# Optimization experiments

Hardware: AMD Instinct MI355X
Metric: run time of the kernel (lower is better)

Reference implementation:

```python
import jax, jax.numpy as jnp
import numpy as np

B, D, E = 8192, 4096, 64
TOP_K = 2
NOISE_EPSILON = 0.01


def setup_inputs() -> dict:
    key = jax.random.key(0)
    k1, k2, k3, k4 = jax.random.split(key, 4)
    return {
        "x": jax.random.normal(k1, (B, D), dtype=jnp.float32),
        # nn.Linear weights, init std=0.1, no bias; torch stores [out, in]
        "gate_w": jax.random.normal(k2, (E, D), dtype=jnp.float32) * 0.1,
        "noise_gate_w": jax.random.normal(k3, (E, D), dtype=jnp.float32) * 0.1,
        # deterministic stand-in for torch.randn_like(clean_logits)
        "noise": jax.random.normal(k4, (B, E), dtype=jnp.float32),
    }


def reference(x, gate_w, noise_gate_w, noise):
    # clean_logits = x @ W_g^T : [B, E]
    clean_logits = jnp.einsum("bd,ed->be", x, gate_w)
    # training path: noisy logits with softplus-scaled noise
    noise_logits = jnp.einsum("bd,ed->be", x, noise_gate_w)
    noisy_logits = clean_logits + noise * jax.nn.softplus(noise_logits) * NOISE_EPSILON
    # top-k over experts, softmax over the k selected logits
    top_k_logits, top_k_indices = jax.lax.top_k(noisy_logits, TOP_K)  # [B, k]
    top_k_gates = jax.nn.softmax(top_k_logits, axis=-1)
    # scatter back into dense [B, E] gates
    rows = jnp.arange(noisy_logits.shape[0])[:, None]  # [B, 1]
    gates = jnp.zeros_like(noisy_logits).at[rows, top_k_indices].set(top_k_gates)
    load = jax.nn.softmax(clean_logits, axis=-1)
    return (gates, load)
```

## Files before the change

### kernel.cpp

```cpp
#include <hip/hip_runtime.h>
#include <math.h>

#define BB 8192
#define DD 4096
#define EE 64

constexpr float NOISE_EPS = 0.01f;
constexpr int BM  = 64;
constexpr int BK  = 32;

typedef __attribute__((ext_vector_type(8))) _Float16 f16x8;
typedef __attribute__((ext_vector_type(4))) float    f32x4;

__device__ __forceinline__ void split8(const float4& a, const float4& b,
                                       f16x8& hi, f16x8& mi) {
    float v[8] = {a.x, a.y, a.z, a.w, b.x, b.y, b.z, b.w};
    #pragma unroll
    for (int j = 0; j < 8; ++j) {
        _Float16 h = (_Float16)v[j];
        hi[j] = h;
        mi[j] = (_Float16)(v[j] - (float)h);
    }
}

__device__ __forceinline__ void gl_lds16(const void* g, void* l) {
    __builtin_amdgcn_global_load_lds(
        (const __attribute__((address_space(1))) unsigned*)g,
        (__attribute__((address_space(3))) unsigned*)l, 16, 0, 0);
}

__global__ __launch_bounds__(256) void wsplit_pack(
    const float* __restrict__ gw, const float* __restrict__ ngw,
    char* __restrict__ wpk)
{
    const int gid = blockIdx.x * 256 + threadIdx.x;
    const int r   = gid >> 9;
    const int kc  = gid & 511;
    const int k0  = kc * 8;
    const float* src = (r < EE) ? gw + (size_t)r * DD + k0
                                : ngw + (size_t)(r - EE) * DD + k0;
    float4 a = *reinterpret_cast<const float4*>(src);
    float4 b = *reinterpret_cast<const float4*>(src + 4);
    f16x8 hi, mi;
    split8(a, b, hi, mi);
    const int T    = k0 >> 5;
    const int kq   = (k0 >> 3) & 3;
    const int cb   = r >> 4;
    const int lane = kq * 16 + (r & 15);
    char* base = wpk + (size_t)T * 16384;
    *reinterpret_cast<f16x8*>(base + ((cb * 2 + 0) * 64 + lane) * 16) = hi;
    *reinterpret_cast<f16x8*>(base + ((cb * 2 + 1) * 64 + lane) * 16) = mi;
}

template <int SK>
__global__ __launch_bounds__(512, 4) void gating_main(
    const float* __restrict__ x,
    const char*  __restrict__ wpk,
    float* __restrict__ partial)
{
    constexpr int KC  = DD / SK;
    constexpr int NKS = KC / BK;

    __shared__ __align__(1024) char xbuf[4][8192];

    const int tid  = threadIdx.x;
    const int bid  = blockIdx.x;
    const int sk   = bid & (SK - 1);
    const int row0 = (bid / SK) * BM;
    const int lane = tid & 63;
    const int wv   = tid >> 6;
    const int m2   = wv & 1;
    const int n2   = wv >> 1;
    const int l15  = lane & 15;
    const int kq   = lane >> 4;

    const int xrow = tid >> 3;
    const int xch  = tid & 7;
    const float* xg = x + (size_t)(row0 + xrow) * DD + sk * KC
                        + ((xch ^ (xrow & 7)) << 2);
    const int ldst = wv * 1024;
    char* xls = (char*)&xbuf[0][0];

    int xoff[2][2];
    #pragma unroll
    for (int mb = 0; mb < 2; ++mb) {
        const int ar = m2 * 32 + mb * 16 + l15;
        #pragma unroll
        for (int u = 0; u < 2; ++u)
            xoff[mb][u] = ar * 128 + (((kq * 2 + u) ^ (ar & 7)) << 4);
    }

    const char* wgB = wpk + ((size_t)(sk * NKS) << 14) + lane * 16;
    const int off_h0 = ((n2 * 2 + 0) * 2 + 0) * 1024;
    const int off_m0 = ((n2 * 2 + 0) * 2 + 1) * 1024;
    const int off_h1 = ((n2 * 2 + 1) * 2 + 0) * 1024;
    const int off_m1 = ((n2 * 2 + 1) * 2 + 1) * 1024;

    f32x4 acc00 = {0.f,0.f,0.f,0.f}, acc01 = {0.f,0.f,0.f,0.f};
    f32x4 acc10 = {0.f,0.f,0.f,0.f}, acc11 = {0.f,0.f,0.f,0.f};

    #define LOADB(t, BH0, BM0, BH1, BM1) do {                                  \
        const char* _b = wgB + ((size_t)(t) << 14);                            \
        BH0 = *reinterpret_cast<const f16x8*>(_b + off_h0);                    \
        BM0 = *reinterpret_cast<const f16x8*>(_b + off_m0);                    \
        BH1 = *reinterpret_cast<const f16x8*>(_b + off_h1);                    \
        BM1 = *reinterpret_cast<const f16x8*>(_b + off_m1);                    \
    } while (0)

    #define COMPUTE(t, BH0, BM0, BH1, BM1) do {                                \
        const char* _xb = xls + (((t) & 3) << 13);                             \
        float4 a00 = *reinterpret_cast<const float4*>(_xb + xoff[0][0]);       \
        float4 a01 = *reinterpret_cast<const float4*>(_xb + xoff[0][1]);       \
        float4 a10 = *reinterpret_cast<const float4*>(_xb + xoff[1][0]);       \
        float4 a11 = *reinterpret_cast<const float4*>(_xb + xoff[1][1]);       \
        f16x8 ah0, am0, ah1, am1;                                              \
        split8(a00, a01, ah0, am0);                                            \
        split8(a10, a11, ah1, am1);                                            \
        acc00 = __builtin_amdgcn_mfma_f32_16x16x32_f16(ah0, BH0, acc00, 0,0,0);\
        acc01 = __builtin_amdgcn_mfma_f32_16x16x32_f16(ah0, BH1, acc01, 0,0,0);\
        acc10 = __builtin_amdgcn_mfma_f32_16x16x32_f16(ah1, BH0, acc10, 0,0,0);\
        acc11 = __builtin_amdgcn_mfma_f32_16x16x32_f16(ah1, BH1, acc11, 0,0,0);\
        acc00 = __builtin_amdgcn_mfma_f32_16x16x32_f16(am0, BH0, acc00, 0,0,0);\
        acc01 = __builtin_amdgcn_mfma_f32_16x16x32_f16(am0, BH1, acc01, 0,0,0);\
        acc10 = __builtin_amdgcn_mfma_f32_16x16x32_f16(am1, BH0, acc10, 0,0,0);\
        acc11 = __builtin_amdgcn_mfma_f32_16x16x32_f16(am1, BH1, acc11, 0,0,0);\
        acc00 = __builtin_amdgcn_mfma_f32_16x16x32_f16(ah0, BM0, acc00, 0,0,0);\
        acc01 = __builtin_amdgcn_mfma_f32_16x16x32_f16(ah0, BM1, acc01, 0,0,0);\
        acc10 = __builtin_amdgcn_mfma_f32_16x16x32_f16(ah1, BM0, acc10, 0,0,0);\
        acc11 = __builtin_amdgcn_mfma_f32_16x16x32_f16(ah1, BM1, acc11, 0,0,0);\
    } while (0)

    f16x8 pH0, pM0, pH1, pM1;
    f16x8 qH0, qM0, qH1, qM1;

    gl_lds16(xg,            xls + ldst);
    gl_lds16(xg + BK,       xls + 8192 + ldst);
    gl_lds16(xg + 2 * BK,   xls + 16384 + ldst);
    LOADB(0, pH0, pM0, pH1, pM1);
    asm volatile("s_waitcnt vmcnt(0)" ::: "memory");
    __builtin_amdgcn_s_barrier();

    for (int t = 0; t < NKS; t += 2) {
        {
            const int tb = (t + 1 < NKS) ? t + 1 : NKS - 1;
            LOADB(tb, qH0, qM0, qH1, qM1);
            asm volatile("s_waitcnt vmcnt(5)" ::: "memory");
            __builtin_amdgcn_s_barrier();
            const int tx = (t + 3 < NKS) ? t + 3 : NKS - 1;
            gl_lds16(xg + (size_t)tx * BK, xls + (((t + 3) & 3) << 13) + ldst);
            COMPUTE(t, pH0, pM0, pH1, pM1);
        }
        {
            const int tb = (t + 2 < NKS) ? t + 2 : NKS - 1;
            LOADB(tb, pH0, pM0, pH1, pM1);
            asm volatile("s_waitcnt vmcnt(5)" ::: "memory");
            __builtin_amdgcn_s_barrier();
            const int tx = (t + 4 < NKS) ? t + 4 : NKS - 1;
            gl_lds16(xg + (size_t)tx * BK, xls + (((t + 4) & 3) << 13) + ldst);
            COMPUTE(t + 1, qH0, qM0, qH1, qM1);
        }
    }
    asm volatile("s_waitcnt vmcnt(0)" ::: "memory");

    #undef LOADB
    #undef COMPUTE

    const size_t pbase = ((size_t)sk * BB + row0) * 128;
    #pragma unroll
    for (int j = 0; j < 4; ++j) {
        const int r0 = m2 * 32 + kq * 4 + j;
        const int c0 = n2 * 32 + l15;
        partial[pbase + (size_t)r0 * 128 + c0]             = acc00[j];
        partial[pbase + (size_t)r0 * 128 + c0 + 16]        = acc01[j];
        partial[pbase + (size_t)(r0 + 16) * 128 + c0]      = acc10[j];
        partial[pbase + (size_t)(r0 + 16) * 128 + c0 + 16] = acc11[j];
    }
}

template <int SK>
__global__ __launch_bounds__(512) void gating_epi(
    const float* __restrict__ partial,
    const float* __restrict__ noise,
    float* __restrict__ out)
{
    const int tid  = threadIdx.x;
    const int wv   = tid >> 6;
    const int lane = tid & 63;
    const int l15  = lane & 15;
    const int kq   = lane >> 4;
    const int grow = blockIdx.x * 32 + wv * 4 + kq;
    const int s    = l15;

    const float* pb = partial + (size_t)grow * 128 + 4 * s;
    float4 c4 = {0.f,0.f,0.f,0.f}, n4 = {0.f,0.f,0.f,0.f};
    #pragma unroll
    for (int k = 0; k < SK; ++k) {
        const float* p = pb + (size_t)k * BB * 128;
        float4 a = *reinterpret_cast<const float4*>(p);
        float4 b = *reinterpret_cast<const float4*>(p + 64);
        c4.x += a.x; c4.y += a.y; c4.z += a.z; c4.w += a.w;
        n4.x += b.x; n4.y += b.y; n4.z += b.z; n4.w += b.w;
    }

    float4 nz = *reinterpret_cast<const float4*>(noise + (size_t)grow * EE + 4 * s);

    float cc[4] = {c4.x, c4.y, c4.z, c4.w};
    float nl[4] = {n4.x, n4.y, n4.z, n4.w};
    float m1 = -3.4e38f, m2 = -3.4e38f;
    int   i1 = -1, i2 = -1;
    float cmax = -3.4e38f;
    #pragma unroll
    for (int j = 0; j < 4; ++j) {
        const int e = 4 * s + j;
        float sp  = fmaxf(nl[j], 0.0f) + log1pf(expf(-fabsf(nl[j])));
        float nzj = (j == 0) ? nz.x : (j == 1) ? nz.y : (j == 2) ? nz.z : nz.w;
        float vno = fmaf(nzj * sp, NOISE_EPS, cc[j]);
        if (vno > m1)      { m2 = m1; i2 = i1; m1 = vno; i1 = e; }
        else if (vno > m2) { m2 = vno; i2 = e; }
        cmax = fmaxf(cmax, cc[j]);
    }

    #pragma unroll
    for (int m = 1; m < 16; m <<= 1) {
        float b1 = __shfl_xor(m1, m, 16);
        int  bi1 = __shfl_xor(i1, m, 16);
        float b2 = __shfl_xor(m2, m, 16);
        int  bi2 = __shfl_xor(i2, m, 16);
        cmax = fmaxf(cmax, __shfl_xor(cmax, m, 16));

        bool bwin = (b1 > m1) || (b1 == m1 && bi1 < i1);
        float t1; int ti1; float t2; int ti2;
        if (bwin) {
            t1 = b1; ti1 = bi1;
            bool aw = (m1 > b2) || (m1 == b2 && i1 < bi2);
            t2 = aw ? m1 : b2; ti2 = aw ? i1 : bi2;
        } else {
            t1 = m1; ti1 = i1;
            bool bw = (b1 > m2) || (b1 == m2 && bi1 < i2);
            t2 = bw ? b1 : m2; ti2 = bw ? bi1 : i2;
        }
        m1 = t1; i1 = ti1; m2 = t2; i2 = ti2;
    }

    float tq = expf(m2 - m1);
    float p1 = 1.0f / (1.0f + tq);
    float p2 = tq * p1;

    float e0 = expf(cc[0] - cmax);
    float e1 = expf(cc[1] - cmax);
    float e2 = expf(cc[2] - cmax);
    float e3 = expf(cc[3] - cmax);
    float sum = e0 + e1 + e2 + e3;
    #pragma unroll
    for (int m = 1; m < 16; m <<= 1) sum += __shfl_xor(sum, m, 16);
    float inv = 1.0f / sum;

    const int eb = 4 * s;
    float4 gt;
    gt.x = (eb     == i1) ? p1 : (eb     == i2) ? p2 : 0.0f;
    gt.y = (eb + 1 == i1) ? p1 : (eb + 1 == i2) ? p2 : 0.0f;
    gt.z = (eb + 2 == i1) ? p1 : (eb + 2 == i2) ? p2 : 0.0f;
    gt.w = (eb + 3 == i1) ? p1 : (eb + 3 == i2) ? p2 : 0.0f;
    float4 ld = {e0 * inv, e1 * inv, e2 * inv, e3 * inv};

    *reinterpret_cast<float4*>(out + (size_t)grow * EE + eb) = gt;
    *reinterpret_cast<float4*>(out + (size_t)BB * EE + (size_t)grow * EE + eb) = ld;
}

extern "C" void kernel_launch(void* const* d_in, const int* in_sizes, int n_in,
                              void* d_out, int out_size, void* d_ws, size_t ws_size,
                              hipStream_t stream) {
    const float* x     = (const float*)d_in[0];
    const float* gw    = (const float*)d_in[1];
    const float* ngw   = (const float*)d_in[2];
    const float* noise = (const float*)d_in[3];
    float* out = (float*)d_out;

    char*  wpk     = (char*)d_ws;
    float* partial = (float*)(wpk + (size_t)2 * 1024 * 1024);

    const size_t MB = 1024 * 1024;

    hipLaunchKernelGGL(wsplit_pack, dim3(256), dim3(256), 0, stream, gw, ngw, wpk);

    if (ws_size >= 18 * MB) {
        hipLaunchKernelGGL(gating_main<4>, dim3((BB / BM) * 4), dim3(512), 0, stream,
                           x, wpk, partial);
        hipLaunchKernelGGL(gating_epi<4>, dim3(BB / 32), dim3(512), 0, stream,
                           partial, noise, out);
    } else if (ws_size >= 10 * MB) {
        hipLaunchKernelGGL(gating_main<2>, dim3((BB / BM) * 2), dim3(512), 0, stream,
                           x, wpk, partial);
        hipLaunchKernelGGL(gating_epi<2>, dim3(BB / 32), dim3(512), 0, stream,
                           partial, noise, out);
    } else {
        hipLaunchKernelGGL(gating_main<1>, dim3(BB / BM), dim3(512), 0, stream,
                           x, wpk, partial);
        hipLaunchKernelGGL(gating_epi<1>, dim3(BB / 32), dim3(512), 0, stream,
                           partial, noise, out);
    }
}
```

Before: 55.20 us.

## Stage 128-wide K chunks in double-buffered LDS with one barrier per chunk

The main GEMM loop now stages x through LDS in 128-element K chunks, using two 32 KB buffers instead of four 8 KB buffers of 32 elements. Each barrier-separated step therefore covers four MFMA sub-steps, so there are four times fewer barriers and waitcnts per unit of work. Weight fragments are prefetched two sub-steps ahead, interleaved inside each chunk. The cost is 64 KB of LDS per block, which can limit how many blocks fit per CU, and a coarser prefetch granularity.

```diff
diff --git a/kernel.cpp b/kernel.cpp
--- a/kernel.cpp
+++ b/kernel.cpp
@@ -6,10 +6,10 @@
 #define EE 64
 
 constexpr float NOISE_EPS = 0.01f;
-constexpr int BM  = 64;
-constexpr int BK  = 32;
+constexpr int BM = 64;
 
 typedef __attribute__((ext_vector_type(8))) _Float16 f16x8;
+typedef __attribute__((ext_vector_type(2))) _Float16 f16x2;
 typedef __attribute__((ext_vector_type(4))) float    f32x4;
 
 __device__ __forceinline__ void split8(const float4& a, const float4& b,
@@ -58,10 +58,11 @@
     const char*  __restrict__ wpk,
     float* __restrict__ partial)
 {
-    constexpr int KC  = DD / SK;
-    constexpr int NKS = KC / BK;
-
-    __shared__ __align__(1024) char xbuf[4][8192];
+    constexpr int KC   = DD / SK;
+    constexpr int NKS  = KC / 128;
+    constexpr int GMAX = 4 * NKS - 1;
+
+    __shared__ __align__(1024) char xls_[2][32768];
 
     const int tid  = threadIdx.x;
     const int bid  = blockIdx.x;
@@ -74,96 +75,98 @@
     const int l15  = lane & 15;
     const int kq   = lane >> 4;
 
-    const int xrow = tid >> 3;
-    const int xch  = tid & 7;
-    const float* xg = x + (size_t)(row0 + xrow) * DD + sk * KC
-                        + ((xch ^ (xrow & 7)) << 2);
-    const int ldst = wv * 1024;
-    char* xls = (char*)&xbuf[0][0];
-
-    int xoff[2][2];
+    const int r_ = tid >> 3, s_ = tid & 7;
+    const float* xg = x + (size_t)(row0 + r_) * DD + sk * KC
+                        + ((s_ ^ (r_ & 7)) << 2);
+
+    int aoff[2][2];
     #pragma unroll
     for (int mb = 0; mb < 2; ++mb) {
         const int ar = m2 * 32 + mb * 16 + l15;
         #pragma unroll
         for (int u = 0; u < 2; ++u)
-            xoff[mb][u] = ar * 128 + (((kq * 2 + u) ^ (ar & 7)) << 4);
-    }
-
-    const char* wgB = wpk + ((size_t)(sk * NKS) << 14) + lane * 16;
-    const int off_h0 = ((n2 * 2 + 0) * 2 + 0) * 1024;
-    const int off_m0 = ((n2 * 2 + 0) * 2 + 1) * 1024;
-    const int off_h1 = ((n2 * 2 + 1) * 2 + 0) * 1024;
-    const int off_m1 = ((n2 * 2 + 1) * 2 + 1) * 1024;
+            aoff[mb][u] = ar * 128 + (((kq * 2 + u) ^ (ar & 7)) << 4);
+    }
+
+    const char* wpkB = wpk + ((size_t)(sk * NKS * 4) << 14) + lane * 16;
+    const int oh0 = ((n2 * 2 + 0) * 2 + 0) * 1024;
+    const int om0 = ((n2 * 2 + 0) * 2 + 1) * 1024;
+    const int oh1 = ((n2 * 2 + 1) * 2 + 0) * 1024;
+    const int om1 = ((n2 * 2 + 1) * 2 + 1) * 1024;
 
     f32x4 acc00 = {0.f,0.f,0.f,0.f}, acc01 = {0.f,0.f,0.f,0.f};
     f32x4 acc10 = {0.f,0.f,0.f,0.f}, acc11 = {0.f,0.f,0.f,0.f};
 
-    #define LOADB(t, BH0, BM0, BH1, BM1) do {                                  \
-        const char* _b = wgB + ((size_t)(t) << 14);                            \
-        BH0 = *reinterpret_cast<const f16x8*>(_b + off_h0);                    \
-        BM0 = *reinterpret_cast<const f16x8*>(_b + off_m0);                    \
-        BH1 = *reinterpret_cast<const f16x8*>(_b + off_h1);                    \
-        BM1 = *reinterpret_cast<const f16x8*>(_b + off_m1);                    \
+    #define LOADB(g, H0, M0, H1, M1) do {                                      \
+        const char* _b = wpkB + ((size_t)(g) << 14);                           \
+        H0 = *reinterpret_cast<const f16x8*>(_b + oh0);                        \
+        M0 = *reinterpret_cast<const f16x8*>(_b + om0);                        \
+        H1 = *reinterpret_cast<const f16x8*>(_b + oh1);                        \
+        M1 = *reinterpret_cast<const f16x8*>(_b + om1);                        \
     } while (0)
 
-    #define COMPUTE(t, BH0, BM0, BH1, BM1) do {                                \
-        const char* _xb = xls + (((t) & 3) << 13);                             \
-        float4 a00 = *reinterpret_cast<const float4*>(_xb + xoff[0][0]);       \
-        float4 a01 = *reinterpret_cast<const float4*>(_xb + xoff[0][1]);       \
-        float4 a10 = *reinterpret_cast<const float4*>(_xb + xoff[1][0]);       \
-        float4 a11 = *reinterpret_cast<const float4*>(_xb + xoff[1][1]);       \
+    #define CHUNK(c, H0, M0, H1, M1) do {                                      \
+        const char* _xb = bufc + (c) * 8192;                                   \
+        float4 a00 = *reinterpret_cast<const float4*>(_xb + aoff[0][0]);       \
+        float4 a01 = *reinterpret_cast<const float4*>(_xb + aoff[0][1]);       \
+        float4 a10 = *reinterpret_cast<const float4*>(_xb + aoff[1][0]);       \
+        float4 a11 = *reinterpret_cast<const float4*>(_xb + aoff[1][1]);       \
         f16x8 ah0, am0, ah1, am1;                                              \
         split8(a00, a01, ah0, am0);                                            \
         split8(a10, a11, ah1, am1);                                            \
-        acc00 = __builtin_amdgcn_mfma_f32_16x16x32_f16(ah0, BH0, acc00, 0,0,0);\
-        acc01 = __builtin_amdgcn_mfma_f32_16x16x32_f16(ah0, BH1, acc01, 0,0,0);\
-        acc10 = __builtin_amdgcn_mfma_f32_16x16x32_f16(ah1, BH0, acc10, 0,0,0);\
-        acc11 = __builtin_amdgcn_mfma_f32_16x16x32_f16(ah1, BH1, acc11, 0,0,0);\
-        acc00 = __builtin_amdgcn_mfma_f32_16x16x32_f16(am0, BH0, acc00, 0,0,0);\
-        acc01 = __builtin_amdgcn_mfma_f32_16x16x32_f16(am0, BH1, acc01, 0,0,0);\
-        acc10 = __builtin_amdgcn_mfma_f32_16x16x32_f16(am1, BH0, acc10, 0,0,0);\
-        acc11 = __builtin_amdgcn_mfma_f32_16x16x32_f16(am1, BH1, acc11, 0,0,0);\
-        acc00 = __builtin_amdgcn_mfma_f32_16x16x32_f16(ah0, BM0, acc00, 0,0,0);\
-        acc01 = __builtin_amdgcn_mfma_f32_16x16x32_f16(ah0, BM1, acc01, 0,0,0);\
-        acc10 = __builtin_amdgcn_mfma_f32_16x16x32_f16(ah1, BM0, acc10, 0,0,0);\
-        acc11 = __builtin_amdgcn_mfma_f32_16x16x32_f16(ah1, BM1, acc11, 0,0,0);\
+        acc00 = __builtin_amdgcn_mfma_f32_16x16x32_f16(ah0, H0, acc00, 0,0,0); \
+        acc01 = __builtin_amdgcn_mfma_f32_16x16x32_f16(ah0, H1, acc01, 0,0,0); \
+        acc10 = __builtin_amdgcn_mfma_f32_16x16x32_f16(ah1, H0, acc10, 0,0,0); \
+        acc11 = __builtin_amdgcn_mfma_f32_16x16x32_f16(ah1, H1, acc11, 0,0,0); \
+        acc00 = __builtin_amdgcn_mfma_f32_16x16x32_f16(am0, H0, acc00, 0,0,0); \
+        acc01 = __builtin_amdgcn_mfma_f32_16x16x32_f16(am0, H1, acc01, 0,0,0); \
+        acc10 = __builtin_amdgcn_mfma_f32_16x16x32_f16(am1, H0, acc10, 0,0,0); \
+        acc11 = __builtin_amdgcn_mfma_f32_16x16x32_f16(am1, H1, acc11, 0,0,0); \
+        acc00 = __builtin_amdgcn_mfma_f32_16x16x32_f16(ah0, M0, acc00, 0,0,0); \
+        acc01 = __builtin_amdgcn_mfma_f32_16x16x32_f16(ah0, M1, acc01, 0,0,0); \
+        acc10 = __builtin_amdgcn_mfma_f32_16x16x32_f16(ah1, M0, acc10, 0,0,0); \
+        acc11 = __builtin_amdgcn_mfma_f32_16x16x32_f16(ah1, M1, acc11, 0,0,0); \
+        { const int _g = 4 * t + (c) + 2;                                      \
+          LOADB((_g <= GMAX) ? _g : GMAX, H0, M0, H1, M1); }                   \
     } while (0)
 
-    f16x8 pH0, pM0, pH1, pM1;
-    f16x8 qH0, qM0, qH1, qM1;
-
-    gl_lds16(xg,            xls + ldst);
-    gl_lds16(xg + BK,       xls + 8192 + ldst);
-    gl_lds16(xg + 2 * BK,   xls + 16384 + ldst);
-    LOADB(0, pH0, pM0, pH1, pM1);
+    f16x8 p0, p1, p2, p3;
+    f16x8 q0, q1, q2, q3;
+
+    {
+        char* d = xls_[0] + wv * 1024;
+        gl_lds16(xg,      d);
+        gl_lds16(xg + 32, d + 8192);
+        gl_lds16(xg + 64, d + 16384);
+        gl_lds16(xg + 96, d + 24576);
+    }
+    LOADB(0, p0, p1, p2, p3);
+    LOADB(1, q0, q1, q2, q3);
+
+    for (int t = 0; t < NKS; ++t) {
+        asm volatile("s_waitcnt vmcnt(8)" ::: "memory");
+        __builtin_amdgcn_s_barrier();
+
+        {
+            const int tn = (t + 1 < NKS) ? t + 1 : t;
+            const float* s = xg + (size_t)tn * 128;
+            char* d = xls_[(t + 1) & 1] + wv * 1024;
+            gl_lds16(s,      d);
+            gl_lds16(s + 32, d + 8192);
+            gl_lds16(s + 64, d + 16384);
+            gl_lds16(s + 96, d + 24576);
+        }
+
+        const char* bufc = xls_[t & 1];
+        CHUNK(0, p0, p1, p2, p3);
+        CHUNK(1, q0, q1, q2, q3);
+        CHUNK(2, p0, p1, p2, p3);
+        CHUNK(3, q0, q1, q2, q3);
+    }
     asm volatile("s_waitcnt vmcnt(0)" ::: "memory");
-    __builtin_amdgcn_s_barrier();
-
-    for (int t = 0; t < NKS; t += 2) {
-        {
-            const int tb = (t + 1 < NKS) ? t + 1 : NKS - 1;
-            LOADB(tb, qH0, qM0, qH1, qM1);
-            asm volatile("s_waitcnt vmcnt(5)" ::: "memory");
-            __builtin_amdgcn_s_barrier();
-            const int tx = (t + 3 < NKS) ? t + 3 : NKS - 1;
-            gl_lds16(xg + (size_t)tx * BK, xls + (((t + 3) & 3) << 13) + ldst);
-            COMPUTE(t, pH0, pM0, pH1, pM1);
-        }
-        {
-            const int tb = (t + 2 < NKS) ? t + 2 : NKS - 1;
-            LOADB(tb, pH0, pM0, pH1, pM1);
-            asm volatile("s_waitcnt vmcnt(5)" ::: "memory");
-            __builtin_amdgcn_s_barrier();
-            const int tx = (t + 4 < NKS) ? t + 4 : NKS - 1;
-            gl_lds16(xg + (size_t)tx * BK, xls + (((t + 4) & 3) << 13) + ldst);
-            COMPUTE(t + 1, qH0, qM0, qH1, qM1);
-        }
-    }
-    asm volatile("s_waitcnt vmcnt(0)" ::: "memory");
 
     #undef LOADB
-    #undef COMPUTE
+    #undef CHUNK
 
     const size_t pbase = ((size_t)sk * BB + row0) * 128;
     #pragma unroll
```

Result: no change. 55.63 us (+0.8%).
